# Performance work log

Hardware: AMD Instinct MI355X
Metric: run time of the kernel (lower is better)

The kernel has to match this reference:

```python
import jax, jax.numpy as jnp
import numpy as np

B, D, M, H, K = 2048, 512, 32768, 4, 64
HD = D // H  # head_dim = 128


def setup_inputs() -> dict:
    key = jax.random.key(0)
    ks = jax.random.split(key, 10)
    s = 1.0 / np.sqrt(D)
    return {
        "query": jax.random.normal(ks[0], (B, D), jnp.float32),
        "memory": jax.random.normal(ks[1], (M, D), jnp.float32),
        "Wq": jax.random.normal(ks[2], (D, D), jnp.float32) * s,
        "bq": jax.random.normal(ks[3], (D,), jnp.float32) * s,
        "Wk": jax.random.normal(ks[4], (D, D), jnp.float32) * s,
        "bk": jax.random.normal(ks[5], (D,), jnp.float32) * s,
        "Wv": jax.random.normal(ks[6], (D, D), jnp.float32) * s,
        "bv": jax.random.normal(ks[7], (D,), jnp.float32) * s,
        "Wo": jax.random.normal(ks[8], (D, D), jnp.float32) * s,
        "bo": jax.random.normal(ks[9], (D,), jnp.float32) * s,
        "k": K,
    }


def reference(query, memory, Wq, bq, Wk, bk, Wv, bv, Wo, bo, k):
    # Linear projections (torch nn.Linear: x @ W.T + b)
    Q = (query @ Wq.T + bq).reshape(B, H, HD)      # [B, H, hd]
    Kp = (memory @ Wk.T + bk).reshape(M, H, HD)    # [M, H, hd]
    V = (memory @ Wv.T + bv).reshape(M, H, HD)     # [M, H, hd]

    scores = jnp.einsum('bhd,mhd->bhm', Q, Kp) / jnp.sqrt(jnp.float32(HD))  # [B, H, M]

    # top-k retrieval over the memory axis
    topk_scores, topk_idx = jax.lax.top_k(scores, k)          # [B, H, k]
    weights = jax.nn.softmax(topk_scores, axis=-1)            # [B, H, k]

    # gather V per head: V_topk[b,h,n,:] = V[topk_idx[b,h,n], h, :]
    Vt = jnp.transpose(V, (1, 0, 2))                          # [H, M, hd]
    V_topk = Vt[jnp.arange(H)[None, :, None], topk_idx]       # [B, H, k, hd]

    attended = jnp.einsum('bhk,bhkd->bhd', weights, V_topk)   # [B, H, hd]
    attended = attended.reshape(B, D)
    return attended @ Wo.T + bo
```

## Files before the change

### kernel.cpp

```cpp
#include <hip/hip_runtime.h>
#include <hip/hip_bf16.h>
#include <stdint.h>

#define B_  2048
#define D_  512
#define M_  32768
#define H_  4
#define HD_ 128
#define K_  64
#define MS_ 8
#define SLICE_ (M_ / MS_)
#define CH_ 128
#define ROWS_ 32
#define T_  12

typedef __attribute__((ext_vector_type(8))) short short8;
typedef __attribute__((ext_vector_type(4))) float float4v;
typedef __attribute__((ext_vector_type(2))) float float2v;

__device__ __forceinline__ ushort f2bf_rne(float f) {
  union { float f; unsigned u; } c; c.f = f;
  unsigned r = (c.u + 0x7fffu + ((c.u >> 16) & 1u)) >> 16;
  return (ushort)r;
}
__device__ __forceinline__ float bf2f(ushort u) {
  union { unsigned u; float f; } c; c.u = ((unsigned)u) << 16;
  return c.f;
}
__device__ __forceinline__ uint32_t make_key(float s, int inv) {
  union { float f; unsigned u; } c; c.f = s;
  unsigned bf = (c.u + 0x7fffu + ((c.u >> 16) & 1u)) >> 16;
  unsigned s16 = (bf ^ ((bf >> 15) ? 0xFFFFu : 0x8000u)) & 0xFFFFu;
  return (s16 << 13) | (unsigned)inv;
}

__global__ __launch_bounds__(256) void gemm_nt_bias(
    const float* __restrict__ X, const float* __restrict__ W,
    const float* __restrict__ bias, float* __restrict__ C, int N,
    ushort* __restrict__ Cbf) {
  __shared__ float As[16][132];
  __shared__ float Bs[16][132];
  const int t  = threadIdx.x;
  const int tx = t & 15, ty = t >> 4;
  const int rowbase = blockIdx.x * 128;
  const int colbase = blockIdx.y * 128;
  float2v acc2[8][4];
  #pragma unroll
  for (int i = 0; i < 8; ++i)
    #pragma unroll
    for (int j = 0; j < 4; ++j) acc2[i][j] = (float2v){0.f, 0.f};

  float4 va[2], vw[2];
  auto gload = [&](int k0) {
    #pragma unroll
    for (int i = 0; i < 2; ++i) {
      int idx = t + i * 256;
      int r = idx >> 2, kq = idx & 3;
      va[i] = *(const float4*)&X[(size_t)(rowbase + r) * 512 + k0 + kq * 4];
      vw[i] = *(const float4*)&W[(size_t)(colbase + r) * 512 + k0 + kq * 4];
    }
  };
  auto sstore = [&]() {
    #pragma unroll
    for (int i = 0; i < 2; ++i) {
      int idx = t + i * 256;
      int r = idx >> 2, kq = idx & 3;
      As[kq*4+0][r] = va[i].x; As[kq*4+1][r] = va[i].y;
      As[kq*4+2][r] = va[i].z; As[kq*4+3][r] = va[i].w;
      Bs[kq*4+0][r] = vw[i].x; Bs[kq*4+1][r] = vw[i].y;
      Bs[kq*4+2][r] = vw[i].z; Bs[kq*4+3][r] = vw[i].w;
    }
  };

  gload(0);
  for (int k0 = 0; k0 < 512; k0 += 16) {
    sstore();
    __syncthreads();
    if (k0 + 16 < 512) gload(k0 + 16);
    #pragma unroll
    for (int k = 0; k < 16; ++k) {
      float a[8], b[8];
      *(float4*)&a[0] = *(const float4*)&As[k][ty*8];
      *(float4*)&a[4] = *(const float4*)&As[k][ty*8+4];
      *(float4*)&b[0] = *(const float4*)&Bs[k][tx*8];
      *(float4*)&b[4] = *(const float4*)&Bs[k][tx*8+4];
      const float2v* a2 = (const float2v*)a;
      const float2v* b2 = (const float2v*)b;
      #pragma unroll
      for (int i2 = 0; i2 < 4; ++i2) {
        #pragma unroll
        for (int j = 0; j < 4; ++j) {
          asm("v_pk_fma_f32 %0, %1, %2, %0 op_sel:[0,0,0] op_sel_hi:[0,1,1]"
              : "+v"(acc2[2*i2][j]) : "v"(a2[i2]), "v"(b2[j]));
          asm("v_pk_fma_f32 %0, %1, %2, %0 op_sel:[1,0,0] op_sel_hi:[1,1,1]"
              : "+v"(acc2[2*i2+1][j]) : "v"(a2[i2]), "v"(b2[j]));
        }
      }
    }
    __syncthreads();
  }
  const int hh = colbase >> 7;
  #pragma unroll
  for (int i = 0; i < 8; ++i) {
    size_t r = (size_t)(rowbase + ty*8 + i);
    #pragma unroll
    for (int j4 = 0; j4 < 2; ++j4) {
      int c = colbase + tx*8 + j4*4;
      float4 bv = *(const float4*)&bias[c];
      float4 o;
      o.x = acc2[i][j4*2+0][0] + bv.x;
      o.y = acc2[i][j4*2+0][1] + bv.y;
      o.z = acc2[i][j4*2+1][0] + bv.z;
      o.w = acc2[i][j4*2+1][1] + bv.w;
      *(float4*)&C[r * 512 + c] = o;
      if (Cbf) {
        ushort u[4] __attribute__((aligned(8)));
        u[0] = f2bf_rne(o.x); u[1] = f2bf_rne(o.y);
        u[2] = f2bf_rne(o.z); u[3] = f2bf_rne(o.w);
        const int dd = tx * 8 + j4 * 4;
        *(ushort4*)&Cbf[((size_t)hh * N + r) * 128 + dd] = *(ushort4*)u;
      }
    }
  }
}

__global__ __launch_bounds__(256) void split_w(
    const float* __restrict__ W, ushort* __restrict__ W1,
    ushort* __restrict__ W2) {
  const int i = (blockIdx.x * 256 + threadIdx.x) * 4;
  float4 v = *(const float4*)&W[i];
  float x[4] = {v.x, v.y, v.z, v.w};
  ushort u1[4] __attribute__((aligned(8)));
  ushort u2[4] __attribute__((aligned(8)));
  #pragma unroll
  for (int j = 0; j < 4; ++j) {
    u1[j] = f2bf_rne(x[j]);
    u2[j] = f2bf_rne(x[j] - bf2f(u1[j]));
  }
  *(ushort4*)&W1[i] = *(ushort4*)u1;
  *(ushort4*)&W2[i] = *(ushort4*)u2;
}

__global__ __launch_bounds__(256, 4) void gemm_split_nt(
    const float* __restrict__ X, const ushort* __restrict__ W1,
    const ushort* __restrict__ W2, const float* __restrict__ bias,
    float* __restrict__ C, int N) {
  const int t = threadIdx.x, w = t >> 6, lane = t & 63;
  const int l15 = lane & 15, l4 = lane >> 4;
  const int nb = blockIdx.x * 128 + w * 32;
  const int ob = blockIdx.y * 128;
  const short* w1s = (const short*)W1;
  const short* w2s = (const short*)W2;

  float4v acc[2][8];
  #pragma unroll
  for (int nt = 0; nt < 2; ++nt)
    #pragma unroll
    for (int ot = 0; ot < 8; ++ot) acc[nt][ot] = (float4v){0.f, 0.f, 0.f, 0.f};

  for (int ks = 0; ks < 16; ++ks) {
    short8 x1[2], x2[2];
    #pragma unroll
    for (int nt = 0; nt < 2; ++nt) {
      const float* xp = X + (size_t)(nb + nt * 16 + l15) * 512 + ks * 32 + l4 * 8;
      float xv[8];
      *(float4*)&xv[0] = *(const float4*)xp;
      *(float4*)&xv[4] = *(const float4*)(xp + 4);
      #pragma unroll
      for (int j = 0; j < 8; ++j) {
        ushort hi = f2bf_rne(xv[j]);
        ((ushort*)&x1[nt])[j] = hi;
        ((ushort*)&x2[nt])[j] = f2bf_rne(xv[j] - bf2f(hi));
      }
    }
    #pragma unroll
    for (int ot = 0; ot < 8; ++ot) {
      const size_t wo = (size_t)(ob + ot * 16 + l15) * 512 + ks * 32 + l4 * 8;
      short8 wf1 = *(const short8*)(w1s + wo);
      short8 wf2 = *(const short8*)(w2s + wo);
      #pragma unroll
      for (int nt = 0; nt < 2; ++nt) {
        acc[nt][ot] = __builtin_amdgcn_mfma_f32_16x16x32_bf16(wf1, x1[nt], acc[nt][ot], 0, 0, 0);
        acc[nt][ot] = __builtin_amdgcn_mfma_f32_16x16x32_bf16(wf2, x1[nt], acc[nt][ot], 0, 0, 0);
        acc[nt][ot] = __builtin_amdgcn_mfma_f32_16x16x32_bf16(wf1, x2[nt], acc[nt][ot], 0, 0, 0);
      }
    }
  }

  #pragma unroll
  for (int nt = 0; nt < 2; ++nt) {
    const size_t row = (size_t)(nb + nt * 16 + l15);
    #pragma unroll
    for (int ot = 0; ot < 8; ++ot) {
      const int col = ob + ot * 16 + l4 * 4;
      float4 bv = *(const float4*)&bias[col];
      float4 o;
      o.x = acc[nt][ot][0] + bv.x;
      o.y = acc[nt][ot][1] + bv.y;
      o.z = acc[nt][ot][2] + bv.z;
      o.w = acc[nt][ot][3] + bv.w;
      *(float4*)&C[row * 512 + col] = o;
    }
  }
}

__global__ __launch_bounds__(256, 4) void scores_topk_ll(
    const ushort* __restrict__ Qbf, const ushort* __restrict__ Kbf,
    uint32_t* __restrict__ tkp) {
  const int t = threadIdx.x, w = t >> 6, lane = t & 63;
  const int l   = blockIdx.x;
  const int xcd = l & 7;
  const int i2  = l >> 3;
  const int s   = xcd + 8 * (i2 >> 6);
  const int h   = s >> 3, z = s & 7;
  const int rowbase = (i2 & 63) * ROWS_;
  const int mbase = z * SLICE_;
  const int l15 = lane & 15, l4 = lane >> 4;

  short8 qf0[4], qf1[4];
  {
    const short* Q0 = (const short*)Qbf +
        ((size_t)h * B_ + rowbase + l15) * 128 + l4 * 8;
    const short* Q1 = (const short*)Qbf +
        ((size_t)h * B_ + rowbase + 16 + l15) * 128 + l4 * 8;
    #pragma unroll
    for (int ks = 0; ks < 4; ++ks) {
      qf0[ks] = *(const short8*)(Q0 + ks * 32);
      qf1[ks] = *(const short8*)(Q1 + ks * 32);
    }
  }

  const short* Kh = (const short*)Kbf + (size_t)h * M_ * 128;

  uint32_t kt0[T_], kt1[T_];
  #pragma unroll
  for (int j = 0; j < T_; ++j) { kt0[j] = 0u; kt1[j] = 0u; }

  auto ins = [&](uint32_t c, uint32_t* kt) {
    uint32_t prev = kt[0];
    kt[0] = (kt[0] >= c) ? kt[0] : c;
    #pragma unroll
    for (int i = 1; i < T_; ++i) {
      uint32_t cur = kt[i];
      uint32_t nv;
      asm("v_med3_u32 %0, %1, %2, %3" : "=v"(nv) : "v"(prev), "v"(cur), "v"(c));
      kt[i] = nv;
      prev = cur;
    }
  };

  for (int ch = 0; ch < SLICE_ / CH_; ++ch) {
    const int mb = mbase + ch * CH_;
    short8 buf[8];
    #pragma unroll
    for (int tt = 0; tt < 2; ++tt) {
      const short* Ka = Kh + (size_t)(mb + 32 * w + 16 * tt + l15) * 128 + l4 * 8;
      #pragma unroll
      for (int ks = 0; ks < 4; ++ks)
        buf[tt * 4 + ks] = *(const short8*)(Ka + ks * 32);
    }
    #pragma unroll
    for (int tt = 0; tt < 2; ++tt) {
      const int inv0 = SLICE_ - 1 - (ch * CH_ + 32 * w + 16 * tt + 4 * l4);
      float4v a0 = {0.f, 0.f, 0.f, 0.f};
      float4v a1 = {0.f, 0.f, 0.f, 0.f};
      #pragma unroll
      for (int ks = 0; ks < 4; ++ks) {
        a0 = __builtin_amdgcn_mfma_f32_16x16x32_bf16(buf[tt * 4 + ks], qf0[ks], a0, 0, 0, 0);
        a1 = __builtin_amdgcn_mfma_f32_16x16x32_bf16(buf[tt * 4 + ks], qf1[ks], a1, 0, 0, 0);
      }
      #pragma unroll
      for (int reg = 0; reg < 4; ++reg) ins(make_key(a0[reg], inv0 - reg), kt0);
      #pragma unroll
      for (int reg = 0; reg < 4; ++reg) ins(make_key(a1[reg], inv0 - reg), kt1);
    }
  }

  const int id = w * 4 + l4;
  const size_t base0 =
      ((((size_t)(rowbase + l15)) * H_ + h) * MS_ + z) * (16 * T_) + (size_t)id * T_;
  const size_t base1 =
      ((((size_t)(rowbase + 16 + l15)) * H_ + h) * MS_ + z) * (16 * T_) + (size_t)id * T_;
  #pragma unroll
  for (int j = 0; j < T_; ++j) {
    tkp[base0 + j] = kt0[j];
    tkp[base1 + j] = kt1[j];
  }
}

__global__ __launch_bounds__(256) void topk_select(
    const uint32_t* __restrict__ tkp, int* __restrict__ tki) {
  __shared__ unsigned h1[256];
  __shared__ unsigned h2[256];
  __shared__ unsigned bstar, cstar, nabove;
  __shared__ int ocnt;
  __shared__ int outi[256];
  const int t = threadIdx.x;
  const int bh = blockIdx.x;
  const uint32_t* src = tkp + (size_t)bh * (MS_ * 16 * T_);
  uint32_t k[6];
  #pragma unroll
  for (int j = 0; j < 6; ++j) k[j] = src[j * 256 + t];
  h1[t] = 0; h2[t] = 0;
  if (t == 0) ocnt = 0;
  __syncthreads();
  #pragma unroll
  for (int j = 0; j < 6; ++j) atomicAdd(&h1[k[j] >> 24], 1u);
  __syncthreads();
  unsigned v = h1[t];
  for (int d = 1; d < 256; d <<= 1) {
    unsigned o = (t + d < 256) ? h1[t + d] : 0u;
    __syncthreads();
    v += o; h1[t] = v;
    __syncthreads();
  }
  if (h1[t] >= 64u && (t == 255 || h1[t + 1] < 64u)) {
    bstar = (unsigned)t; nabove = (t == 255) ? 0u : h1[t + 1];
  }
  __syncthreads();
  const unsigned bs = bstar, na = nabove;
  #pragma unroll
  for (int j = 0; j < 6; ++j)
    if ((k[j] >> 24) == bs) atomicAdd(&h2[(k[j] >> 16) & 0xFFu], 1u);
  __syncthreads();
  v = h2[t];
  for (int d = 1; d < 256; d <<= 1) {
    unsigned o = (t + d < 256) ? h2[t + d] : 0u;
    __syncthreads();
    v += o; h2[t] = v;
    __syncthreads();
  }
  if (na + h2[t] >= 64u && (t == 255 || na + h2[t + 1] < 64u)) cstar = (unsigned)t;
  __syncthreads();
  const uint32_t theta = ((((bs << 8) | cstar) << 16)) - 65536u;
  #pragma unroll
  for (int j = 0; j < 6; ++j) {
    if (k[j] >= theta) {
      int p = atomicAdd(&ocnt, 1);
      if (p < 256) {
        const int pos = j * 256 + t;
        const int z = pos / (16 * T_);
        const int ci = (SLICE_ - 1) - (int)(k[j] & 0x1FFFu);
        outi[p] = (z << 12) | ci;
      }
    }
  }
  __syncthreads();
  int n = ocnt; if (n > 256) n = 256;
  if (t >= n) outi[t] = -(t + 1);
  __syncthreads();
  tki[(size_t)bh * 256 + t] = outi[t];
}

__global__ __launch_bounds__(256) void rescore_attend(
    const float* __restrict__ Qp, const float* __restrict__ Kp,
    const float* __restrict__ Vp, const int* __restrict__ tki,
    float* __restrict__ att) {
  __shared__ float q_[128];
  __shared__ float s_[256];
  __shared__ int   i_[256];
  __shared__ float wsm[64];
  __shared__ int   widx[64];
  const int bh = blockIdx.x, b = bh >> 2, h = bh & 3;
  const int t = threadIdx.x, w = t >> 6, lane = t & 63;
  const float SCALE = 0.08838834764831843f;

  if (t < 32) *(float4*)&q_[t * 4] = *(const float4*)&Qp[(size_t)b * 512 + h * 128 + t * 4];
  i_[t] = tki[(size_t)bh * 256 + t];
  __syncthreads();

  const int o = lane >> 3, il = lane & 7;
  #pragma unroll 2
  for (int p = 0; p < 8; ++p) {
    const int j = w * 64 + p * 8 + o;
    const int idx = i_[j];
    const float* kr = Kp + (size_t)(idx < 0 ? 0 : idx) * 512 + h * 128;
    float part = 0.f;
    #pragma unroll
    for (int u = 0; u < 4; ++u) {
      const int f = il + u * 8;
      float4 kv = *(const float4*)&kr[f * 4];
      float4 qv = *(const float4*)&q_[f * 4];
      part += kv.x * qv.x + kv.y * qv.y + kv.z * qv.z + kv.w * qv.w;
    }
    part += __shfl_xor(part, 1);
    part += __shfl_xor(part, 2);
    part += __shfl_xor(part, 4);
    if (il == 0) s_[j] = (idx < 0) ? -3.0e38f : part * SCALE;
  }
  __syncthreads();

  for (int k = 2; k <= 256; k <<= 1) {
    for (int j = k >> 1; j > 0; j >>= 1) {
      if (t < 128) {
        const int i = ((t & ~(j - 1)) << 1) | (t & (j - 1));
        const int p2 = i | j;
        const bool dir = ((i & k) == 0);
        float sa = s_[i], sb = s_[p2];
        int   ia = i_[i], ib = i_[p2];
        const bool inorder = (sa > sb) || (sa == sb && ia <= ib);
        if (inorder != dir) { s_[i] = sb; s_[p2] = sa; i_[i] = ib; i_[p2] = ia; }
      }
      __syncthreads();
    }
  }

  if (t < 64) {
    float sv = s_[t];
    float mx = sv;
    #pragma unroll
    for (int off = 32; off; off >>= 1) mx = fmaxf(mx, __shfl_xor(mx, off));
    float e = expf(sv - mx);
    float zz = e;
    #pragma unroll
    for (int off = 32; off; off >>= 1) zz += __shfl_xor(zz, off);
    wsm[t] = e / zz;
    widx[t] = i_[t];
  }
  __syncthreads();

  if (t < 128) {
    float a = 0.f;
    #pragma unroll 4
    for (int k2 = 0; k2 < 64; ++k2)
      a = fmaf(wsm[k2], Vp[(size_t)widx[k2] * 512 + h * 128 + t], a);
    att[(size_t)b * 512 + h * 128 + t] = a;
  }
}

extern "C" void kernel_launch(void* const* d_in, const int* in_sizes, int n_in,
                              void* d_out, int out_size, void* d_ws, size_t ws_size,
                              hipStream_t stream) {
  const float* query  = (const float*)d_in[0];
  const float* memory = (const float*)d_in[1];
  const float* Wq = (const float*)d_in[2];
  const float* bq = (const float*)d_in[3];
  const float* Wk = (const float*)d_in[4];
  const float* bk = (const float*)d_in[5];
  const float* Wv = (const float*)d_in[6];
  const float* bv = (const float*)d_in[7];
  const float* Wo = (const float*)d_in[8];
  const float* bo = (const float*)d_in[9];
  float* out = (float*)d_out;

  float*  Qp  = (float*)d_ws;
  float*  Kp  = Qp + (size_t)B_ * D_;
  float*  Vp  = Kp + (size_t)M_ * D_;
  int*    tki = (int*)(Vp + (size_t)M_ * D_);
  ushort* Qbf = (ushort*)(tki + (size_t)B_ * H_ * 256);
  ushort* Kbf = Qbf + (size_t)H_ * B_ * 128;
  uint32_t* tkp = (uint32_t*)Vp;
  float*  att = (float*)Kbf;
  ushort* w1v = Kbf + (size_t)2 * 1024 * 1024;
  ushort* w2v = w1v + (size_t)D_ * D_;

  gemm_nt_bias<<<dim3(B_ / 128, 4), 256, 0, stream>>>(query,  Wq, bq, Qp, B_, Qbf);
  gemm_nt_bias<<<dim3(M_ / 128, 4), 256, 0, stream>>>(memory, Wk, bk, Kp, M_, Kbf);

  scores_topk_ll<<<dim3(2048), 256, 0, stream>>>(Qbf, Kbf, tkp);
  topk_select<<<dim3(B_ * H_), 256, 0, stream>>>(tkp, tki);

  split_w<<<dim3(256), 256, 0, stream>>>(Wv, w1v, w2v);
  gemm_split_nt<<<dim3(M_ / 128, 4), 256, 0, stream>>>(memory, w1v, w2v, bv, Vp, M_);

  rescore_attend<<<dim3(B_ * H_), 256, 0, stream>>>(Qp, Kp, Vp, tki, att);

  gemm_nt_bias<<<dim3(B_ / 128, 4), 256, 0, stream>>>(att, Wo, bo, out, B_, nullptr);
}
```

Before: 870.9 us.

## Shrink per-slice topk candidates, simplify key packing, add 64-row GEMM for small projections

Reduces the number of candidates kept per slice in the partial top-k from 12 to 8, shrinking the tkp buffer and the select kernel's work. Key construction drops the bf16 rounding step and takes the truncated upper bits of the sign-flipped float directly. A new 64-row tiled GEMM is used for the query and output projections to launch more blocks for the B-sized matrices. Fewer candidates risks dropping true top-k entries before rescoring.

```diff
diff --git a/kernel.cpp b/kernel.cpp
--- a/kernel.cpp
+++ b/kernel.cpp
@@ -12,7 +12,7 @@
 #define SLICE_ (M_ / MS_)
 #define CH_ 128
 #define ROWS_ 32
-#define T_  12
+#define T_  8
 
 typedef __attribute__((ext_vector_type(8))) short short8;
 typedef __attribute__((ext_vector_type(4))) float float4v;
@@ -29,9 +29,8 @@
 }
 __device__ __forceinline__ uint32_t make_key(float s, int inv) {
   union { float f; unsigned u; } c; c.f = s;
-  unsigned bf = (c.u + 0x7fffu + ((c.u >> 16) & 1u)) >> 16;
-  unsigned s16 = (bf ^ ((bf >> 15) ? 0xFFFFu : 0x8000u)) & 0xFFFFu;
-  return (s16 << 13) | (unsigned)inv;
+  unsigned m = c.u ^ ((unsigned)(((int)c.u) >> 31) | 0x80000000u);
+  return ((m >> 16) << 13) | (unsigned)inv;
 }
 
 __global__ __launch_bounds__(256) void gemm_nt_bias(
@@ -124,6 +123,90 @@
   }
 }
 
+__global__ __launch_bounds__(256) void gemm_nt_bias64(
+    const float* __restrict__ X, const float* __restrict__ W,
+    const float* __restrict__ bias, float* __restrict__ C, int N,
+    ushort* __restrict__ Cbf) {
+  __shared__ float As[16][68];
+  __shared__ float Bs[16][132];
+  const int t  = threadIdx.x;
+  const int tx = t & 15, ty = t >> 4;
+  const int rowbase = blockIdx.x * 64;
+  const int colbase = blockIdx.y * 128;
+  float acc[4][8];
+  #pragma unroll
+  for (int i = 0; i < 4; ++i)
+    #pragma unroll
+    for (int j = 0; j < 8; ++j) acc[i][j] = 0.f;
+
+  float4 va, vw[2];
+  auto gload = [&](int k0) {
+    { int r = t >> 2, kq = t & 3;
+      va = *(const float4*)&X[(size_t)(rowbase + r) * 512 + k0 + kq * 4]; }
+    #pragma unroll
+    for (int i = 0; i < 2; ++i) {
+      int idx = t + i * 256;
+      int r = idx >> 2, kq = idx & 3;
+      vw[i] = *(const float4*)&W[(size_t)(colbase + r) * 512 + k0 + kq * 4];
+    }
+  };
+  auto sstore = [&]() {
+    { int r = t >> 2, kq = t & 3;
+      As[kq*4+0][r] = va.x; As[kq*4+1][r] = va.y;
+      As[kq*4+2][r] = va.z; As[kq*4+3][r] = va.w; }
+    #pragma unroll
+    for (int i = 0; i < 2; ++i) {
+      int idx = t + i * 256;
+      int r = idx >> 2, kq = idx & 3;
+      Bs[kq*4+0][r] = vw[i].x; Bs[kq*4+1][r] = vw[i].y;
+      Bs[kq*4+2][r] = vw[i].z; Bs[kq*4+3][r] = vw[i].w;
+    }
+  };
+
+  gload(0);
+  for (int k0 = 0; k0 < 512; k0 += 16) {
+    sstore();
+    __syncthreads();
+    if (k0 + 16 < 512) gload(k0 + 16);
+    #pragma unroll
+    for (int k = 0; k < 16; ++k) {
+      float a[4], b[8];
+      *(float4*)&a[0] = *(const float4*)&As[k][ty*4];
+      *(float4*)&b[0] = *(const float4*)&Bs[k][tx*8];
+      *(float4*)&b[4] = *(const float4*)&Bs[k][tx*8+4];
+      #pragma unroll
+      for (int i = 0; i < 4; ++i)
+        #pragma unroll
+        for (int j = 0; j < 8; ++j)
+          acc[i][j] = fmaf(a[i], b[j], acc[i][j]);
+    }
+    __syncthreads();
+  }
+  const int hh = colbase >> 7;
+  #pragma unroll
+  for (int i = 0; i < 4; ++i) {
+    size_t r = (size_t)(rowbase + ty*4 + i);
+    #pragma unroll
+    for (int j4 = 0; j4 < 2; ++j4) {
+      int c = colbase + tx*8 + j4*4;
+      float4 bv = *(const float4*)&bias[c];
+      float4 o;
+      o.x = acc[i][j4*4+0] + bv.x;
+      o.y = acc[i][j4*4+1] + bv.y;
+      o.z = acc[i][j4*4+2] + bv.z;
+      o.w = acc[i][j4*4+3] + bv.w;
+      *(float4*)&C[r * 512 + c] = o;
+      if (Cbf) {
+        ushort u[4] __attribute__((aligned(8)));
+        u[0] = f2bf_rne(o.x); u[1] = f2bf_rne(o.y);
+        u[2] = f2bf_rne(o.z); u[3] = f2bf_rne(o.w);
+        const int dd = tx * 8 + j4 * 4;
+        *(ushort4*)&Cbf[((size_t)hh * N + r) * 128 + dd] = *(ushort4*)u;
+      }
+    }
+  }
+}
+
 __global__ __launch_bounds__(256) void split_w(
     const float* __restrict__ W, ushort* __restrict__ W1,
     ushort* __restrict__ W2) {
@@ -298,14 +381,14 @@
   const int t = threadIdx.x;
   const int bh = blockIdx.x;
   const uint32_t* src = tkp + (size_t)bh * (MS_ * 16 * T_);
-  uint32_t k[6];
-  #pragma unroll
-  for (int j = 0; j < 6; ++j) k[j] = src[j * 256 + t];
+  uint32_t k[4];
+  #pragma unroll
+  for (int j = 0; j < 4; ++j) k[j] = src[j * 256 + t];
   h1[t] = 0; h2[t] = 0;
   if (t == 0) ocnt = 0;
   __syncthreads();
   #pragma unroll
-  for (int j = 0; j < 6; ++j) atomicAdd(&h1[k[j] >> 24], 1u);
+  for (int j = 0; j < 4; ++j) atomicAdd(&h1[k[j] >> 24], 1u);
   __syncthreads();
   unsigned v = h1[t];
   for (int d = 1; d < 256; d <<= 1) {
@@ -320,7 +403,7 @@
   __syncthreads();
   const unsigned bs = bstar, na = nabove;
   #pragma unroll
-  for (int j = 0; j < 6; ++j)
+  for (int j = 0; j < 4; ++j)
     if ((k[j] >> 24) == bs) atomicAdd(&h2[(k[j] >> 16) & 0xFFu], 1u);
   __syncthreads();
   v = h2[t];
@@ -334,13 +417,13 @@
   __syncthreads();
   const uint32_t theta = ((((bs << 8) | cstar) << 16)) - 65536u;
   #pragma unroll
-  for (int j = 0; j < 6; ++j) {
+  for (int j = 0; j < 4; ++j) {
     if (k[j] >= theta) {
       int p = atomicAdd(&ocnt, 1);
       if (p < 256) {
         const int pos = j * 256 + t;
-        const int z = pos / (16 * T_);
-        const int ci = (SLICE_ - 1) - (int)(k[j] & 0x1FFFu);
+        const int z = pos >> 7;
+        const int ci = (SLICE_ - 1) - (int)(k[j] & 0xFFFu);
         outi[p] = (z << 12) | ci;
       }
     }
@@ -454,7 +537,7 @@
   ushort* w1v = Kbf + (size_t)2 * 1024 * 1024;
   ushort* w2v = w1v + (size_t)D_ * D_;
 
-  gemm_nt_bias<<<dim3(B_ / 128, 4), 256, 0, stream>>>(query,  Wq, bq, Qp, B_, Qbf);
+  gemm_nt_bias64<<<dim3(B_ / 64, 4), 256, 0, stream>>>(query, Wq, bq, Qp, B_, Qbf);
   gemm_nt_bias<<<dim3(M_ / 128, 4), 256, 0, stream>>>(memory, Wk, bk, Kp, M_, Kbf);
 
   scores_topk_ll<<<dim3(2048), 256, 0, stream>>>(Qbf, Kbf, tkp);
@@ -465,5 +548,5 @@
 
   rescore_attend<<<dim3(B_ * H_), 256, 0, stream>>>(Qp, Kp, Vp, tki, att);
 
-  gemm_nt_bias<<<dim3(B_ / 128, 4), 256, 0, stream>>>(att, Wo, bo, out, B_, nullptr);
-}
+  gemm_nt_bias64<<<dim3(B_ / 64, 4), 256, 0, stream>>>(att, Wo, bo, out, B_, nullptr);
+}
```

Result: faster. 826.8 us (-5.1%).
